# Kernel tuning notes

Measured on AMD Instinct MI355X. Metric: run time of the kernel, lower is better.

Reference implementation:

```python
import jax, jax.numpy as jnp
import numpy as np

E = 32          # num_experts
K = 4           # num_experts_per_tok
H = 1024        # hidden_size
I = 768         # moe_intermediate_size
ROUTED_SCALING_FACTOR = 1.0


def setup_inputs() -> dict:
    key = jax.random.key(0)
    k0, k1, k2, k3, k4, k5 = jax.random.split(key, 6)
    return {
        "hidden_states": jax.random.normal(k0, (1, 2048, H), jnp.float32),
        "gate_w": jax.random.normal(k1, (E, H), jnp.float32) * 0.02,
        "w1": jax.random.normal(k2, (E, H, I), jnp.float32) * 0.02,   # gate proj per expert
        "w3": jax.random.normal(k3, (E, H, I), jnp.float32) * 0.02,   # up proj per expert
        "w2": jax.random.normal(k4, (E, I, H), jnp.float32) * 0.02,   # down proj per expert
        "e_bias": jax.random.normal(k5, (E,), jnp.float32) * 0.02,    # e_score_correction_bias
    }


def reference(hidden_states, gate_w, w1, w3, w2, e_bias):
    orig_shape = hidden_states.shape
    x = hidden_states.reshape(-1, orig_shape[-1])            # [T, H]
    T = x.shape[0]

    # ----- router gate (ReplicatedLinear, no bias) -----
    router_logits = x @ gate_w.T                             # [T, E]

    # ----- grouped top-k with num_expert_group=1, topk_group=1 == plain top-k
    # scoring_func='sigmoid'; correction bias only affects expert *selection*,
    # the routing weights are the uncorrected sigmoid scores.
    scores = jax.nn.sigmoid(router_logits.astype(jnp.float32))          # [T, E]
    _, topk_ids = jax.lax.top_k(scores + e_bias[None, :], K)            # [T, K]
    topk_w = jnp.take_along_axis(scores, topk_ids, axis=1)              # [T, K]
    # renormalize (norm_topk_prob=True)
    topk_w = topk_w / jnp.sum(topk_w, axis=1, keepdims=True)

    # dense combine weights [T, E] (zero for unselected experts)
    combine = jnp.zeros((T, E), jnp.float32).at[jnp.arange(T)[:, None], topk_ids].add(topk_w)

    # ----- experts: SwiGLU per expert, combine weighted -----
    g = jnp.einsum("th,ehi->tei", x, w1)                     # [T, E, I]
    u = jnp.einsum("th,ehi->tei", x, w3)                     # [T, E, I]
    a = jax.nn.silu(g) * u * combine[:, :, None].astype(x.dtype)
    out = jnp.einsum("tei,eih->th", a, w2)                   # [T, H]

    out = out * ROUTED_SCALING_FACTOR
    return out.reshape(orig_shape)
```

## Files before the change

kernel.cpp:

```cpp
#include <hip/hip_runtime.h>
#include <cstdint>

#define TOK 2048
#define HD  1024
#define ID  768
#define NE  32
#define BM  320
#define NPOS (TOK * 4)

typedef unsigned short u16t;
typedef unsigned int   u32t;
typedef __bf16 bf16x8 __attribute__((ext_vector_type(8)));
typedef float  f32x4  __attribute__((ext_vector_type(4)));
typedef u16t   u16x8  __attribute__((ext_vector_type(8)));
typedef u16t   u16x4  __attribute__((ext_vector_type(4)));
typedef float  fvec4  __attribute__((ext_vector_type(4)));

__device__ __forceinline__ u16t f2b(float f) {
  u32t u = __float_as_uint(f);
  u32t r = u + 0x7fffu + ((u >> 16) & 1u);
  return (u16t)(r >> 16);
}

#define BAR() do { \
    asm volatile("s_waitcnt lgkmcnt(0)" ::: "memory"); \
    __builtin_amdgcn_s_barrier(); \
    __builtin_amdgcn_sched_barrier(0); \
  } while (0)

__global__ void k_router(const float* __restrict__ x, const float* __restrict__ gw,
                         const float* __restrict__ eb,
                         int* __restrict__ topk_ids, float* __restrict__ topk_w,
                         int* __restrict__ counts) {
  int lane = threadIdx.x & 63;
  int t = blockIdx.x * 4 + (threadIdx.x >> 6);
  const float* xt = x + (size_t)t * HD;
  fvec4 xr[4];
#pragma unroll
  for (int i = 0; i < 4; ++i) xr[i] = *(const fvec4*)(xt + lane * 4 + i * 256);
  float myscore = 0.f;
  for (int e = 0; e < NE; ++e) {
    const float* ge = gw + (size_t)e * HD + lane * 4;
    float s = 0.f;
#pragma unroll
    for (int i = 0; i < 4; ++i) {
      fvec4 g = *(const fvec4*)(ge + i * 256);
      s = fmaf(xr[i][0], g[0], s); s = fmaf(xr[i][1], g[1], s);
      s = fmaf(xr[i][2], g[2], s); s = fmaf(xr[i][3], g[3], s);
    }
#pragma unroll
    for (int off = 32; off; off >>= 1) s += __shfl_xor(s, off);
    if (lane == e) myscore = s;
  }
  float sig = 1.f / (1.f + expf(-myscore));
  float biased = (lane < NE) ? (sig + eb[lane]) : -3.0e38f;
  float wsum = 0.f;
  int ids[4]; float wsv[4];
#pragma unroll
  for (int k = 0; k < 4; ++k) {
    float v = biased; int idx = lane;
#pragma unroll
    for (int off = 32; off; off >>= 1) {
      float ov = __shfl_xor(v, off);
      int   oi = __shfl_xor(idx, off);
      if (ov > v || (ov == v && oi < idx)) { v = ov; idx = oi; }
    }
    ids[k] = idx;
    float sc = __shfl(sig, idx);
    wsv[k] = sc; wsum += sc;
    if (lane == idx) biased = -3.0e38f;
  }
  float inv = 1.f / wsum;
#pragma unroll
  for (int k = 0; k < 4; ++k) {
    if (lane == k) {
      topk_ids[t * 4 + k] = ids[k];
      topk_w[t * 4 + k]  = wsv[k] * inv;
      atomicAdd(&counts[ids[k]], 1);
    }
  }
}

__global__ void k_bucket(const int* __restrict__ topk_ids, const float* __restrict__ topk_w,
                         const int* __restrict__ counts, int* __restrict__ offsets,
                         int* __restrict__ pairTok, float* __restrict__ pairW,
                         int* __restrict__ invp) {
  __shared__ int soff[NE + 1];
  __shared__ int scur[NE];
  int tid = threadIdx.x;
  if (tid == 0) {
    int acc = 0;
    for (int e = 0; e < NE; ++e) { soff[e] = acc; acc += counts[e]; }
    soff[NE] = acc;
  }
  if (tid < NE) scur[tid] = 0;
  __syncthreads();
  if (tid <= NE) offsets[tid] = soff[tid];
  for (int p = tid; p < NPOS; p += 256) {
    int e = topk_ids[p];
    int pos = soff[e] + atomicAdd(&scur[e], 1);
    pairTok[pos] = p;
    pairW[pos]   = topk_w[p];
    invp[p]      = pos;
  }
}

__global__ void k_permute(const float* __restrict__ x, const int* __restrict__ pairTok,
                          u16t* __restrict__ Xp) {
  const int c = blockIdx.x;
  const int t = threadIdx.x;
  const int r = t & 15;
  const int tok = pairTok[c * 16 + r] >> 2;
  const float* xrow = x + (size_t)tok * HD;
  u16t* outp = Xp + (size_t)c * 16384;
#pragma unroll
  for (int i = 0; i < 8; ++i) {
    int G = t + i * 256;
    int s = G >> 6, g = (G >> 4) & 3;
    const float* src = xrow + s * 32 + g * 8;
    fvec4 a = *(const fvec4*)src, b = *(const fvec4*)(src + 4);
    u16x8 o = { f2b(a[0]), f2b(a[1]), f2b(a[2]), f2b(a[3]),
                f2b(b[0]), f2b(b[1]), f2b(b[2]), f2b(b[3]) };
    *(u16x8*)&outp[(size_t)G * 8] = o;
  }
}

__launch_bounds__(256, 3)
__global__ void k_gemm1(const u16t* __restrict__ Xp, const float* __restrict__ w1,
                        const float* __restrict__ w3,
                        const int* __restrict__ counts, const int* __restrict__ offsets,
                        const float* __restrict__ pairW,
                        u16t* __restrict__ A) {
  const int e = blockIdx.y;
  const int colbase = blockIdx.x * 32;
  const int count = counts[e];
  const int base  = offsets[e];
  const int tid = threadIdx.x, lane = tid & 63, wv = tid >> 6;
  const int l15 = lane & 15, kcl = lane >> 4;

  __shared__ __align__(16) u16t Ws[2][2][1024];
  __shared__ float pw[BM];

  const int mat_s = tid >> 7;
  const int v = tid & 127;
  const int wcolL = v & 31;
  const int kcs = v >> 5;
  const float* wp = (mat_s ? w3 : w1) + (size_t)e * HD * ID
                    + (size_t)(kcs * 8) * ID + colbase + wcolL;

#define G1_AFLOAD(AF, S) do { \
    _Pragma("unroll") for (int q = 0; q < 5; ++q) \
      AF[q] = *(const u16x8*)((const char*)Xp + xsrc[q] + (u32t)(S) * 1024u); \
  } while (0)
#define G1_WLOAD(KB) do { \
    _Pragma("unroll") for (int j = 0; j < 8; ++j) \
      wd[j] = wp[(size_t)((KB) + j) * ID]; \
  } while (0)
#define G1_WSTORE(P) do { \
    u16x8 pk = { f2b(wd[0]), f2b(wd[1]), f2b(wd[2]), f2b(wd[3]), \
                 f2b(wd[4]), f2b(wd[5]), f2b(wd[6]), f2b(wd[7]) }; \
    *(u16x8*)&Ws[P][mat_s][kcs * 256 + wcolL * 8] = pk; \
  } while (0)
#define G1_MFMA(AF, P) do { \
    _Pragma("unroll") for (int m = 0; m < 2; ++m) \
      _Pragma("unroll") for (int cf = 0; cf < 2; ++cf) { \
        bf16x8 b = *(const bf16x8*)&Ws[P][m][kcl * 256 + (cf * 16 + l15) * 8]; \
        _Pragma("unroll") for (int rf = 0; rf < 5; ++rf) \
          acc[rf][cf][m] = __builtin_amdgcn_mfma_f32_16x16x32_bf16(AF[rf], b, acc[rf][cf][m], 0, 0, 0); \
      } \
  } while (0)

  for (int r0 = 0; r0 < count; r0 += BM) {
    __syncthreads();
    {
      int i = r0 + tid;
      pw[tid] = (i < count) ? pairW[base + i] : 0.f;
      if (tid < BM - 256) {
        int i2 = r0 + 256 + tid;
        pw[256 + tid] = (i2 < count) ? pairW[base + i2] : 0.f;
      }
    }
    u32t xsrc[5];
#pragma unroll
    for (int q = 0; q < 5; ++q) {
      int pos = base + r0 + wv * 80 + q * 16 + l15;
      pos = pos < NPOS ? pos : NPOS - 1;
      xsrc[q] = (u32t)(pos >> 4) * 32768u + (u32t)kcl * 256u + (u32t)(pos & 15) * 16u;
    }

    f32x4 zz = {0.f, 0.f, 0.f, 0.f};
    f32x4 acc[5][2][2];
#pragma unroll
    for (int a = 0; a < 5; ++a)
#pragma unroll
      for (int b = 0; b < 2; ++b) { acc[a][b][0] = zz; acc[a][b][1] = zz; }

    u16x8 afA[5], afB[5];
    float wd[8];
    G1_AFLOAD(afA, 0);
    G1_AFLOAD(afB, 1);
    G1_WLOAD(0);
    G1_WSTORE(0);
    G1_WLOAD(32);
    BAR();

    for (int s = 0; s < 32; s += 2) {
      G1_WSTORE(1);
      { const int k2 = (s + 2 < 32) ? s + 2 : 31; G1_WLOAD(k2 * 32); }
      G1_MFMA(afA, 0);
      { const int s2 = (s + 2 < 32) ? s + 2 : 31; G1_AFLOAD(afA, s2); }
      BAR();
      G1_WSTORE(0);
      { const int k3 = (s + 3 < 32) ? s + 3 : 31; G1_WLOAD(k3 * 32); }
      G1_MFMA(afB, 1);
      { const int s3 = (s + 3 < 32) ? s + 3 : 31; G1_AFLOAD(afB, s3); }
      BAR();
    }

    const u32t bx512 = (u32t)blockIdx.x * 512u;
#pragma unroll
    for (int rf = 0; rf < 5; ++rf)
#pragma unroll
      for (int ri = 0; ri < 4; ++ri) {
        int row = wv * 80 + rf * 16 + (lane >> 4) * 4 + ri;
        int grow = r0 + row;
        if (grow < count) {
          float wgt = pw[row];
          int pos = base + grow;
          u32t rbase = (u32t)(pos >> 4) * 12288u + bx512 + (u32t)(pos & 15) * 8u;
#pragma unroll
          for (int cf = 0; cf < 2; ++cf) {
            float gg = acc[rf][cf][0][ri];
            float uu = acc[rf][cf][1][ri];
            float a = gg / (1.f + expf(-gg)) * uu * wgt;
            int cc = cf * 16 + l15;
            A[rbase + (u32t)((cc >> 3) & 3) * 128u + (u32t)(cc & 7)] = f2b(a);
          }
        }
      }
  }
#undef G1_AFLOAD
#undef G1_WLOAD
#undef G1_WSTORE
#undef G1_MFMA
}

__launch_bounds__(256, 4)
__global__ void k_gemm2(const u16t* __restrict__ Ab, const float* __restrict__ w2,
                        const int* __restrict__ counts, const int* __restrict__ offsets,
                        float* __restrict__ buf) {
  const int e = blockIdx.y;
  const int colbase = blockIdx.x * 32;
  const int count = counts[e];
  const int base  = offsets[e];
  const int tid = threadIdx.x, lane = tid & 63, wv = tid >> 6;
  const int l15 = lane & 15, kcl = lane >> 4;

  __shared__ __align__(16) u16t Ws[2][1024];

  const int wcolL = tid & 31;
  const int h = tid >> 5;
  const float* w2t = w2 + (size_t)e * ID * HD + (size_t)(h * 4) * HD + colbase + wcolL;
  const int wdst = (h >> 1) * 256 + wcolL * 8 + (h & 1) * 4;

#define G2_AFLOAD(AF, S) do { \
    _Pragma("unroll") for (int q = 0; q < 5; ++q) \
      AF[q] = *(const u16x8*)((const char*)Ab + asrc[q] + (u32t)(S) * 1024u); \
  } while (0)
#define G2_WLOAD(KB) do { \
    _Pragma("unroll") for (int j = 0; j < 4; ++j) \
      wd[j] = w2t[(size_t)((KB) + j) * HD]; \
  } while (0)
#define G2_WSTORE(P) do { \
    u16x4 pk = { f2b(wd[0]), f2b(wd[1]), f2b(wd[2]), f2b(wd[3]) }; \
    *(u16x4*)&Ws[P][wdst] = pk; \
  } while (0)
#define G2_MFMA(AF, P) do { \
    _Pragma("unroll") for (int cf = 0; cf < 2; ++cf) { \
      bf16x8 b = *(const bf16x8*)&Ws[P][kcl * 256 + (cf * 16 + l15) * 8]; \
      _Pragma("unroll") for (int rf = 0; rf < 5; ++rf) \
        acc[rf][cf] = __builtin_amdgcn_mfma_f32_16x16x32_bf16(AF[rf], b, acc[rf][cf], 0, 0, 0); \
    } \
  } while (0)

  for (int r0 = 0; r0 < count; r0 += BM) {
    __syncthreads();
    u32t asrc[5];
#pragma unroll
    for (int q = 0; q < 5; ++q) {
      int pos = base + r0 + wv * 80 + q * 16 + l15;
      pos = pos < NPOS ? pos : NPOS - 1;
      asrc[q] = (u32t)(pos >> 4) * 24576u + (u32t)kcl * 256u + (u32t)(pos & 15) * 16u;
    }

    f32x4 zz = {0.f, 0.f, 0.f, 0.f};
    f32x4 acc[5][2];
#pragma unroll
    for (int a = 0; a < 5; ++a) { acc[a][0] = zz; acc[a][1] = zz; }

    u16x8 afA[5], afB[5];
    float wd[4];
    G2_AFLOAD(afA, 0);
    G2_AFLOAD(afB, 1);
    G2_WLOAD(0);
    G2_WSTORE(0);
    G2_WLOAD(32);
    BAR();

    for (int s = 0; s < 24; s += 2) {
      G2_WSTORE(1);
      { const int k2 = (s + 2 < 24) ? s + 2 : 23; G2_WLOAD(k2 * 32); }
      G2_MFMA(afA, 0);
      { const int s2 = (s + 2 < 24) ? s + 2 : 23; G2_AFLOAD(afA, s2); }
      BAR();
      G2_WSTORE(0);
      { const int k3 = (s + 3 < 24) ? s + 3 : 23; G2_WLOAD(k3 * 32); }
      G2_MFMA(afB, 1);
      { const int s3 = (s + 3 < 24) ? s + 3 : 23; G2_AFLOAD(afB, s3); }
      BAR();
    }

#pragma unroll
    for (int rf = 0; rf < 5; ++rf)
#pragma unroll
      for (int ri = 0; ri < 4; ++ri) {
        int row = wv * 80 + rf * 16 + (lane >> 4) * 4 + ri;
        int grow = r0 + row;
        if (grow < count) {
#pragma unroll
          for (int cf = 0; cf < 2; ++cf)
            buf[(size_t)(base + grow) * HD + colbase + cf * 16 + l15] = acc[rf][cf][ri];
        }
      }
  }
#undef G2_AFLOAD
#undef G2_WLOAD
#undef G2_WSTORE
#undef G2_MFMA
}

__global__ void k_reduce(const float* __restrict__ buf, const int* __restrict__ invp,
                         float* __restrict__ out) {
  int t = blockIdx.x;
  int col = threadIdx.x * 4;
  int p0 = invp[t * 4 + 0], p1 = invp[t * 4 + 1];
  int p2 = invp[t * 4 + 2], p3 = invp[t * 4 + 3];
  fvec4 s = *(const fvec4*)(buf + (size_t)p0 * HD + col);
  s += *(const fvec4*)(buf + (size_t)p1 * HD + col);
  s += *(const fvec4*)(buf + (size_t)p2 * HD + col);
  s += *(const fvec4*)(buf + (size_t)p3 * HD + col);
  *(fvec4*)(out + (size_t)t * HD + col) = s;
}

extern "C" void kernel_launch(void* const* d_in, const int* in_sizes, int n_in,
                              void* d_out, int out_size, void* d_ws, size_t ws_size,
                              hipStream_t stream) {
  const float* x  = (const float*)d_in[0];
  const float* gw = (const float*)d_in[1];
  const float* w1 = (const float*)d_in[2];
  const float* w3 = (const float*)d_in[3];
  const float* w2 = (const float*)d_in[4];
  const float* eb = (const float*)d_in[5];
  float* out = (float*)d_out;

  char* ws = (char*)d_ws;
  int*   counts   = (int*)(ws);
  int*   offsets  = (int*)(ws + 256);
  int*   topk_ids = (int*)(ws + 4096);
  float* topk_w   = (float*)(ws + 36864);
  int*   pairTok  = (int*)(ws + 69632);
  float* pairW    = (float*)(ws + 102400);
  int*   invp     = (int*)(ws + 135168);
  u16t*  Xp   = (u16t*)(ws + 262144);
  float* buf  = (float*)(ws + 262144);
  u16t*  Abuf = (u16t*)(ws + 262144 + 33554432);

  hipMemsetAsync(counts, 0, 4096, stream);
  k_router <<<512, 256, 0, stream>>>(x, gw, eb, topk_ids, topk_w, counts);
  k_bucket <<<1, 256, 0, stream>>>(topk_ids, topk_w, counts, offsets, pairTok, pairW, invp);
  k_permute<<<512, 256, 0, stream>>>(x, pairTok, Xp);
  k_gemm1  <<<dim3(24, 32), 256, 0, stream>>>(Xp, w1, w3, counts, offsets, pairW, Abuf);
  k_gemm2  <<<dim3(32, 32), 256, 0, stream>>>(Abuf, w2, counts, offsets, buf);
  k_reduce <<<2048, 256, 0, stream>>>(buf, invp, out);
}
```

Baseline: 239.6 us.

## Vectorize fp32 weight loads and double K-step per barrier stage in both GEMMs

Each thread now loads the fp32 expert weights as float4 vectors covering 4 adjacent columns across several K rows, instead of scalar loads of one column over 8 or 4 rows. The shared-memory tile grows to hold 64 K values per stage, so each barrier pair covers twice as much MFMA work and the number of barriers is halved. Global weight traffic becomes wider and more coalesced per instruction. In exchange, the bf16 shared-memory stores are scattered 32-bit writes that may hit bank conflicts, LDS use doubles, and register pressure rises.

```diff
diff --git a/kernel.cpp b/kernel.cpp
--- a/kernel.cpp
+++ b/kernel.cpp
@@ -138,35 +138,38 @@
   const int tid = threadIdx.x, lane = tid & 63, wv = tid >> 6;
   const int l15 = lane & 15, kcl = lane >> 4;
 
-  __shared__ __align__(16) u16t Ws[2][2][1024];
+  __shared__ __align__(16) u16t Ws[2][2][2][4][256];
   __shared__ float pw[BM];
 
   const int mat_s = tid >> 7;
-  const int v = tid & 127;
-  const int wcolL = v & 31;
-  const int kcs = v >> 5;
-  const float* wp = (mat_s ? w3 : w1) + (size_t)e * HD * ID
-                    + (size_t)(kcs * 8) * ID + colbase + wcolL;
+  const int vv = tid & 127;
+  const int col4 = (vv & 7) * 4;
+  const int kr = vv >> 3;
+  const int wm = kr >> 3, wkc = (kr >> 1) & 3, wob = (kr & 1) * 4;
+  const float* wp = (mat_s ? w3 : w1) + (size_t)e * HD * ID + colbase + col4;
 
 #define G1_AFLOAD(AF, S) do { \
     _Pragma("unroll") for (int q = 0; q < 5; ++q) \
       AF[q] = *(const u16x8*)((const char*)Xp + xsrc[q] + (u32t)(S) * 1024u); \
   } while (0)
-#define G1_WLOAD(KB) do { \
-    _Pragma("unroll") for (int j = 0; j < 8; ++j) \
-      wd[j] = wp[(size_t)((KB) + j) * ID]; \
+#define G1_WLOAD(SS) do { \
+    const float* _s = wp + (size_t)((SS) * 64 + kr * 4) * ID; \
+    wd[0] = *(const fvec4*)_s;            wd[1] = *(const fvec4*)(_s + ID); \
+    wd[2] = *(const fvec4*)(_s + 2 * ID); wd[3] = *(const fvec4*)(_s + 3 * ID); \
   } while (0)
 #define G1_WSTORE(P) do { \
-    u16x8 pk = { f2b(wd[0]), f2b(wd[1]), f2b(wd[2]), f2b(wd[3]), \
-                 f2b(wd[4]), f2b(wd[5]), f2b(wd[6]), f2b(wd[7]) }; \
-    *(u16x8*)&Ws[P][mat_s][kcs * 256 + wcolL * 8] = pk; \
-  } while (0)
-#define G1_MFMA(AF, P) do { \
-    _Pragma("unroll") for (int m = 0; m < 2; ++m) \
+    _Pragma("unroll") for (int c = 0; c < 4; ++c) { \
+      u32t p0 = (u32t)f2b(wd[0][c]) | ((u32t)f2b(wd[1][c]) << 16); \
+      u32t p1 = (u32t)f2b(wd[2][c]) | ((u32t)f2b(wd[3][c]) << 16); \
+      *(u32t*)&Ws[P][mat_s][wm][wkc][(col4 + c) * 8 + wob]     = p0; \
+      *(u32t*)&Ws[P][mat_s][wm][wkc][(col4 + c) * 8 + wob + 2] = p1; \
+    } } while (0)
+#define G1_MFMA(AF, P, M) do { \
+    _Pragma("unroll") for (int m2 = 0; m2 < 2; ++m2) \
       _Pragma("unroll") for (int cf = 0; cf < 2; ++cf) { \
-        bf16x8 b = *(const bf16x8*)&Ws[P][m][kcl * 256 + (cf * 16 + l15) * 8]; \
+        bf16x8 b = *(const bf16x8*)&Ws[P][m2][M][kcl][(cf * 16 + l15) * 8]; \
         _Pragma("unroll") for (int rf = 0; rf < 5; ++rf) \
-          acc[rf][cf][m] = __builtin_amdgcn_mfma_f32_16x16x32_bf16(AF[rf], b, acc[rf][cf][m], 0, 0, 0); \
+          acc[rf][cf][m2] = __builtin_amdgcn_mfma_f32_16x16x32_bf16(AF[rf], b, acc[rf][cf][m2], 0, 0, 0); \
       } \
   } while (0)
 
@@ -196,24 +199,28 @@
       for (int b = 0; b < 2; ++b) { acc[a][b][0] = zz; acc[a][b][1] = zz; }
 
     u16x8 afA[5], afB[5];
-    float wd[8];
+    fvec4 wd[4];
     G1_AFLOAD(afA, 0);
     G1_AFLOAD(afB, 1);
     G1_WLOAD(0);
     G1_WSTORE(0);
-    G1_WLOAD(32);
+    G1_WLOAD(1);
     BAR();
 
-    for (int s = 0; s < 32; s += 2) {
+    for (int ss = 0; ss < 16; ss += 2) {
       G1_WSTORE(1);
-      { const int k2 = (s + 2 < 32) ? s + 2 : 31; G1_WLOAD(k2 * 32); }
-      G1_MFMA(afA, 0);
-      { const int s2 = (s + 2 < 32) ? s + 2 : 31; G1_AFLOAD(afA, s2); }
+      if (ss + 2 < 16) G1_WLOAD(ss + 2);
+      G1_MFMA(afA, 0, 0);
+      { const int n = (2 * ss + 2 < 32) ? 2 * ss + 2 : 31; G1_AFLOAD(afA, n); }
+      G1_MFMA(afB, 0, 1);
+      { const int n = (2 * ss + 3 < 32) ? 2 * ss + 3 : 31; G1_AFLOAD(afB, n); }
       BAR();
       G1_WSTORE(0);
-      { const int k3 = (s + 3 < 32) ? s + 3 : 31; G1_WLOAD(k3 * 32); }
-      G1_MFMA(afB, 1);
-      { const int s3 = (s + 3 < 32) ? s + 3 : 31; G1_AFLOAD(afB, s3); }
+      if (ss + 3 < 16) G1_WLOAD(ss + 3);
+      G1_MFMA(afA, 1, 0);
+      { const int n = (2 * ss + 4 < 32) ? 2 * ss + 4 : 31; G1_AFLOAD(afA, n); }
+      G1_MFMA(afB, 1, 1);
+      { const int n = (2 * ss + 5 < 32) ? 2 * ss + 5 : 31; G1_AFLOAD(afB, n); }
       BAR();
     }
 
@@ -256,28 +263,29 @@
   const int tid = threadIdx.x, lane = tid & 63, wv = tid >> 6;
   const int l15 = lane & 15, kcl = lane >> 4;
 
-  __shared__ __align__(16) u16t Ws[2][1024];
-
-  const int wcolL = tid & 31;
-  const int h = tid >> 5;
-  const float* w2t = w2 + (size_t)e * ID * HD + (size_t)(h * 4) * HD + colbase + wcolL;
-  const int wdst = (h >> 1) * 256 + wcolL * 8 + (h & 1) * 4;
+  __shared__ __align__(16) u16t Ws[2][2][4][256];
+
+  const int col4 = (tid & 7) * 4;
+  const int kr = tid >> 3;
+  const int wm = kr >> 4, wkc = (kr >> 2) & 3, wob = (kr & 3) * 2;
+  const float* wp = w2 + (size_t)e * ID * HD + colbase + col4;
 
 #define G2_AFLOAD(AF, S) do { \
     _Pragma("unroll") for (int q = 0; q < 5; ++q) \
       AF[q] = *(const u16x8*)((const char*)Ab + asrc[q] + (u32t)(S) * 1024u); \
   } while (0)
-#define G2_WLOAD(KB) do { \
-    _Pragma("unroll") for (int j = 0; j < 4; ++j) \
-      wd[j] = w2t[(size_t)((KB) + j) * HD]; \
+#define G2_WLOAD(SS) do { \
+    const float* _s = wp + (size_t)((SS) * 64 + kr * 2) * HD; \
+    wd[0] = *(const fvec4*)_s; wd[1] = *(const fvec4*)(_s + HD); \
   } while (0)
 #define G2_WSTORE(P) do { \
-    u16x4 pk = { f2b(wd[0]), f2b(wd[1]), f2b(wd[2]), f2b(wd[3]) }; \
-    *(u16x4*)&Ws[P][wdst] = pk; \
-  } while (0)
-#define G2_MFMA(AF, P) do { \
+    _Pragma("unroll") for (int c = 0; c < 4; ++c) { \
+      u32t pk = (u32t)f2b(wd[0][c]) | ((u32t)f2b(wd[1][c]) << 16); \
+      *(u32t*)&Ws[P][wm][wkc][(col4 + c) * 8 + wob] = pk; \
+    } } while (0)
+#define G2_MFMA(AF, P, M) do { \
     _Pragma("unroll") for (int cf = 0; cf < 2; ++cf) { \
-      bf16x8 b = *(const bf16x8*)&Ws[P][kcl * 256 + (cf * 16 + l15) * 8]; \
+      bf16x8 b = *(const bf16x8*)&Ws[P][M][kcl][(cf * 16 + l15) * 8]; \
       _Pragma("unroll") for (int rf = 0; rf < 5; ++rf) \
         acc[rf][cf] = __builtin_amdgcn_mfma_f32_16x16x32_bf16(AF[rf], b, acc[rf][cf], 0, 0, 0); \
     } \
@@ -299,24 +307,28 @@
     for (int a = 0; a < 5; ++a) { acc[a][0] = zz; acc[a][1] = zz; }
 
     u16x8 afA[5], afB[5];
-    float wd[4];
+    fvec4 wd[2];
     G2_AFLOAD(afA, 0);
     G2_AFLOAD(afB, 1);
     G2_WLOAD(0);
     G2_WSTORE(0);
-    G2_WLOAD(32);
+    G2_WLOAD(1);
     BAR();
 
-    for (int s = 0; s < 24; s += 2) {
+    for (int ss = 0; ss < 12; ss += 2) {
       G2_WSTORE(1);
-      { const int k2 = (s + 2 < 24) ? s + 2 : 23; G2_WLOAD(k2 * 32); }
-      G2_MFMA(afA, 0);
-      { const int s2 = (s + 2 < 24) ? s + 2 : 23; G2_AFLOAD(afA, s2); }
+      if (ss + 2 < 12) G2_WLOAD(ss + 2);
+      G2_MFMA(afA, 0, 0);
+      { const int n = (2 * ss + 2 < 24) ? 2 * ss + 2 : 23; G2_AFLOAD(afA, n); }
+      G2_MFMA(afB, 0, 1);
+      { const int n = (2 * ss + 3 < 24) ? 2 * ss + 3 : 23; G2_AFLOAD(afB, n); }
       BAR();
       G2_WSTORE(0);
-      { const int k3 = (s + 3 < 24) ? s + 3 : 23; G2_WLOAD(k3 * 32); }
-      G2_MFMA(afB, 1);
-      { const int s3 = (s + 3 < 24) ? s + 3 : 23; G2_AFLOAD(afB, s3); }
+      if (ss + 3 < 12) G2_WLOAD(ss + 3);
+      G2_MFMA(afA, 1, 0);
+      { const int n = (2 * ss + 4 < 24) ? 2 * ss + 4 : 23; G2_AFLOAD(afA, n); }
+      G2_MFMA(afB, 1, 1);
+      { const int n = (2 * ss + 5 < 24) ? 2 * ss + 5 : 23; G2_AFLOAD(afB, n); }
       BAR();
     }
 
```

New measurement: 322.9 us. +34.8%, slower.
